# Kernel tuning notes

Hardware: AMD Instinct MI355X
Metric: run time of the kernel (lower is better)

The kernel has to match this reference:

```python
import jax, jax.numpy as jnp
import numpy as np

T, B, IN = 64, 4096, 145
H1, H2 = 150, 32


def _lstm_layer(x, w_ih, w_hh, b_ih, b_hh):
    """Single LSTM layer, PyTorch gate order (i, f, g, o).
    x: (T, B, in_dim); w_ih: (4H, in_dim); w_hh: (4H, H); biases: (4H,).
    Returns hidden sequence (T, B, H)."""
    H = w_hh.shape[1]
    Bsz = x.shape[1]
    # Precompute input contribution for all timesteps at once (one big GEMM).
    xg = jnp.einsum('tbi,gi->tbg', x, w_ih) + (b_ih + b_hh)  # (T, B, 4H)
    w_hh_t = w_hh.T  # (H, 4H)

    def step(carry, xg_t):
        h, c = carry
        gates = xg_t + h @ w_hh_t  # (B, 4H)
        i, f, g, o = jnp.split(gates, 4, axis=-1)
        i = jax.nn.sigmoid(i)
        f = jax.nn.sigmoid(f)
        g = jnp.tanh(g)
        o = jax.nn.sigmoid(o)
        c = f * c + i * g
        h = o * jnp.tanh(c)
        return (h, c), h

    h0 = jnp.zeros((Bsz, H), x.dtype)
    c0 = jnp.zeros((Bsz, H), x.dtype)
    _, hs = jax.lax.scan(step, (h0, c0), xg)
    return hs  # (T, B, H)


def _init_lstm_params(key, in_dim, hidden):
    # PyTorch init: U(-k, k) with k = 1/sqrt(hidden)
    k = 1.0 / np.sqrt(hidden)
    ks = jax.random.split(key, 4)
    w_ih = jax.random.uniform(ks[0], (4 * hidden, in_dim), jnp.float32, -k, k)
    w_hh = jax.random.uniform(ks[1], (4 * hidden, hidden), jnp.float32, -k, k)
    b_ih = jax.random.uniform(ks[2], (4 * hidden,), jnp.float32, -k, k)
    b_hh = jax.random.uniform(ks[3], (4 * hidden,), jnp.float32, -k, k)
    return w_ih, w_hh, b_ih, b_hh


def setup_inputs() -> dict:
    key = jax.random.key(0)
    kx, k0, k1, k2 = jax.random.split(key, 4)
    x = jax.random.normal(kx, (T, B, IN), jnp.float32)
    w_ih_l0, w_hh_l0, b_ih_l0, b_hh_l0 = _init_lstm_params(k0, IN, H1)
    w_ih_l1, w_hh_l1, b_ih_l1, b_hh_l1 = _init_lstm_params(k1, H1, H1)
    w_ih_l2, w_hh_l2, b_ih_l2, b_hh_l2 = _init_lstm_params(k2, H1, H2)
    return {
        'x': x,
        'w_ih_l0': w_ih_l0, 'w_hh_l0': w_hh_l0, 'b_ih_l0': b_ih_l0, 'b_hh_l0': b_hh_l0,
        'w_ih_l1': w_ih_l1, 'w_hh_l1': w_hh_l1, 'b_ih_l1': b_ih_l1, 'b_hh_l1': b_hh_l1,
        'w_ih_l2': w_ih_l2, 'w_hh_l2': w_hh_l2, 'b_ih_l2': b_ih_l2, 'b_hh_l2': b_hh_l2,
    }


def reference(x,
              w_ih_l0, w_hh_l0, b_ih_l0, b_hh_l0,
              w_ih_l1, w_hh_l1, b_ih_l1, b_hh_l1,
              w_ih_l2, w_hh_l2, b_ih_l2, b_hh_l2):
    # temporal_model1: 2-layer LSTM (145 -> 150 -> 150)
    h = _lstm_layer(x, w_ih_l0, w_hh_l0, b_ih_l0, b_hh_l0)
    h = _lstm_layer(h, w_ih_l1, w_hh_l1, b_ih_l1, b_hh_l1)
    # temporal_model2: 1-layer LSTM (150 -> 32)
    out2 = _lstm_layer(h, w_ih_l2, w_hh_l2, b_ih_l2, b_hh_l2)
    return out2  # (T, B, 32)
```

## Files before the change

### kernel.cpp

```cpp
#include <hip/hip_runtime.h>


typedef _Float16 f16;
typedef _Float16 f16x8 __attribute__((ext_vector_type(8)));
typedef float f32x4 __attribute__((ext_vector_type(4)));

#define T_STEPS 64
#define BATCH 4096

__device__ __forceinline__ float sigf(float x) { return 1.0f / (1.0f + __expf(-x)); }
__device__ __forceinline__ float tanh_f(float x) {
  float e = __expf(2.0f * x);
  return 1.0f - 2.0f / (e + 1.0f);
}

#define BAR_LGKM() asm volatile("s_waitcnt lgkmcnt(0)\n\ts_barrier" ::: "memory")

#define PIN_FRAG(w) asm volatile("" : "+v"(*reinterpret_cast<f32x4*>(&(w))))

template <int IN_DIM, int H, int MODE>
__global__ __attribute__((amdgpu_waves_per_eu(2, 2))) __launch_bounds__(512) void lstm_layer(
    const float* __restrict__ xin_f32, const f16* __restrict__ xin_f16,
    const float* __restrict__ w_ih, const float* __restrict__ w_hh,
    const float* __restrict__ b_ih, const float* __restrict__ b_hh,
    f16* __restrict__ hout, float* __restrict__ yout) {
  constexpr int KX = (IN_DIM + 31) / 32;
  constexpr int XPAD = KX * 32;
  constexpr int XSTR = XPAD + 8;
  constexpr int KH = (H + 31) / 32;
  constexpr int HSTR = KH * 32 + 8;
  constexpr int NPAD = ((H + 31) / 32) * 32;
  constexpr int NT = NPAD / 32;
  constexpr int GROUPS = NPAD * 4;
  constexpr int UPD_ITERS = (GROUPS + 511) / 512;
  constexpr int XIN_ELEMS = 16 * IN_DIM;
  constexpr int QX = (XIN_ELEMS + 511) / 512;
  constexpr int STG = (16 * XSTR) / 8;
  constexpr int HCP = (16 * HSTR) / 8;
  static_assert(MODE == 0 || XSTR == 168, "ws stride must match LDS stride");
  static_assert(MODE == 2 || HSTR == 168, "h tile must match ws stride");

  __shared__ __align__(16) f16 xbuf[2][16 * XSTR];
  __shared__ __align__(16) f16 hbuf[16 * HSTR];
  __shared__ __align__(16) float gates[NPAD * 84];

  const int tid = threadIdx.x;
  const int l = tid & 63;
  const int wv = tid >> 6;
  const int gate = wv >> 1;
  const int half = wv & 1;
  const int lrow = l & 15;
  const int lk8 = (l >> 4) * 8;
  const int r0 = (l >> 4) * 4;
  const int b0 = blockIdx.x * 16;

  {
    f16* xf = &xbuf[0][0];
    for (int i = tid; i < 2 * 16 * XSTR; i += 512) xf[i] = (f16)0.f;
    for (int i = tid; i < 16 * HSTR; i += 512) hbuf[i] = (f16)0.f;
  }

  const int rbase = half * (NPAD / 2) + lrow;
  float bias_reg[NT];
#pragma unroll
  for (int nt = 0; nt < NT; ++nt) {
    int n = rbase + nt * 16;
    bias_reg[nt] = (n < H) ? (b_ih[gate * H + n] + b_hh[gate * H + n]) : 0.f;
  }

  f16x8 wx[KX][NT], wh[KH][NT];
#pragma unroll
  for (int kc = 0; kc < KX; ++kc)
#pragma unroll
    for (int nt = 0; nt < NT; ++nt) {
      f16x8 w;
#pragma unroll
      for (int j = 0; j < 8; ++j) {
        int k = kc * 32 + lk8 + j;
        int r = rbase + nt * 16;
        float v = (r < H && k < IN_DIM) ? w_ih[(size_t)(gate * H + r) * IN_DIM + k] : 0.f;
        w[j] = (f16)v;
      }
      wx[kc][nt] = w;
      PIN_FRAG(wx[kc][nt]);
    }
#pragma unroll
  for (int kc = 0; kc < KH; ++kc)
#pragma unroll
    for (int nt = 0; nt < NT; ++nt) {
      f16x8 w;
#pragma unroll
      for (int j = 0; j < 8; ++j) {
        int k = kc * 32 + lk8 + j;
        int r = rbase + nt * 16;
        float v = (r < H && k < H) ? w_hh[(size_t)(gate * H + r) * H + k] : 0.f;
        w[j] = (f16)v;
      }
      wh[kc][nt] = w;
      PIN_FRAG(wh[kc][nt]);
    }

  if constexpr (MODE == 0) {
#pragma unroll
    for (int q = 0; q < QX; ++q) {
      int idx = q * 512 + tid;
      if (idx < XIN_ELEMS) {
        float v = xin_f32[(size_t)b0 * IN_DIM + idx];
        int r = idx / IN_DIM, c = idx - r * IN_DIM;
        xbuf[0][r * XSTR + c] = (f16)v;
      }
    }
  } else {
    if (tid < STG) {
      f16x8 v = *(const f16x8*)(xin_f16 + (size_t)b0 * 168 + tid * 8);
      *(f16x8*)(&xbuf[0][tid * 8]) = v;
    }
  }
  __syncthreads();

  float creg[UPD_ITERS][4];
#pragma unroll
  for (int it = 0; it < UPD_ITERS; ++it)
#pragma unroll
    for (int j = 0; j < 4; ++j) creg[it][j] = 0.f;

  float xv[QX];
  f16x8 pv;

  for (int t = 0; t < T_STEPS; ++t) {
    const int cur = t & 1, nxt = cur ^ 1;

    if (t + 1 < T_STEPS) {
      if constexpr (MODE == 0) {
        const float* src = xin_f32 + ((size_t)(t + 1) * BATCH + b0) * IN_DIM;
#pragma unroll
        for (int q = 0; q < QX; ++q) {
          int idx = q * 512 + tid;
          xv[q] = (idx < XIN_ELEMS) ? src[idx] : 0.f;
        }
      } else {
        if (tid < STG)
          pv = *(const f16x8*)(xin_f16 + ((size_t)(t + 1) * BATCH + b0) * 168 + tid * 8);
      }
    }

    if constexpr (MODE != 2) {
      if (t > 0 && tid < HCP) {
        f16x8 v = *(const f16x8*)(&hbuf[tid * 8]);
        *(f16x8*)(hout + ((size_t)(t - 1) * BATCH + b0) * 168 + tid * 8) = v;
      }
    }

    f32x4 acc[NT];
#pragma unroll
    for (int nt = 0; nt < NT; ++nt) {
      float b = bias_reg[nt];
      acc[nt] = f32x4{b, b, b, b};
    }
    {
      const f16* xb = &xbuf[cur][0];
#pragma unroll
      for (int kc = 0; kc < KX; ++kc) {
        f16x8 a = *(const f16x8*)(xb + lrow * XSTR + kc * 32 + lk8);
#pragma unroll
        for (int nt = 0; nt < NT; ++nt)
          acc[nt] = __builtin_amdgcn_mfma_f32_16x16x32_f16(a, wx[kc][nt], acc[nt], 0, 0, 0);
      }
#pragma unroll
      for (int kc = 0; kc < KH; ++kc) {
        f16x8 a = *(const f16x8*)(hbuf + lrow * HSTR + kc * 32 + lk8);
#pragma unroll
        for (int nt = 0; nt < NT; ++nt)
          acc[nt] = __builtin_amdgcn_mfma_f32_16x16x32_f16(a, wh[kc][nt], acc[nt], 0, 0, 0);
      }
    }
#pragma unroll
    for (int nt = 0; nt < NT; ++nt) {
      int n = half * (NPAD / 2) + nt * 16 + lrow;
      *(f32x4*)(&gates[n * 84 + gate * 20 + r0]) = acc[nt];
    }

    BAR_LGKM();

    if (t + 1 < T_STEPS) {
      if constexpr (MODE == 0) {
#pragma unroll
        for (int q = 0; q < QX; ++q) {
          int idx = q * 512 + tid;
          if (idx < XIN_ELEMS) {
            int r = idx / IN_DIM, c = idx - r * IN_DIM;
            xbuf[nxt][r * XSTR + c] = (f16)xv[q];
          }
        }
      } else {
        if (tid < STG) *(f16x8*)(&xbuf[nxt][tid * 8]) = pv;
      }
    }

#pragma unroll
    for (int it = 0; it < UPD_ITERS; ++it) {
      int grp = it * 512 + tid;
      if (grp < GROUPS) {
        int n = grp % NPAD;
        int rb = (grp / NPAD) * 4;
        if (n < H) {
          f32x4 gi = *(const f32x4*)(&gates[n * 84 + 0 + rb]);
          f32x4 gf = *(const f32x4*)(&gates[n * 84 + 20 + rb]);
          f32x4 gg = *(const f32x4*)(&gates[n * 84 + 40 + rb]);
          f32x4 go = *(const f32x4*)(&gates[n * 84 + 60 + rb]);
#pragma unroll
          for (int j = 0; j < 4; ++j) {
            float iv = sigf(gi[j]);
            float fv = sigf(gf[j]);
            float gv = tanh_f(gg[j]);
            float ov = sigf(go[j]);
            float c = fv * creg[it][j] + iv * gv;
            creg[it][j] = c;
            float h = ov * tanh_f(c);
            hbuf[(rb + j) * HSTR + n] = (f16)h;
            if constexpr (MODE == 2) {
              yout[((size_t)t * BATCH + b0 + rb + j) * 32 + n] = h;
            }
          }
        }
      }
    }

    BAR_LGKM();
  }

  if constexpr (MODE != 2) {
    if (tid < HCP) {
      f16x8 v = *(const f16x8*)(&hbuf[tid * 8]);
      *(f16x8*)(hout + ((size_t)(T_STEPS - 1) * BATCH + b0) * 168 + tid * 8) = v;
    }
  }
}

extern "C" void kernel_launch(void* const* d_in, const int* in_sizes, int n_in,
                              void* d_out, int out_size, void* d_ws, size_t ws_size,
                              hipStream_t stream) {
  const float* x = (const float*)d_in[0];
  const float* wih0 = (const float*)d_in[1];
  const float* whh0 = (const float*)d_in[2];
  const float* bih0 = (const float*)d_in[3];
  const float* bhh0 = (const float*)d_in[4];
  const float* wih1 = (const float*)d_in[5];
  const float* whh1 = (const float*)d_in[6];
  const float* bih1 = (const float*)d_in[7];
  const float* bhh1 = (const float*)d_in[8];
  const float* wih2 = (const float*)d_in[9];
  const float* whh2 = (const float*)d_in[10];
  const float* bih2 = (const float*)d_in[11];
  const float* bhh2 = (const float*)d_in[12];

  f16* hws = (f16*)d_ws;
  float* out = (float*)d_out;

  dim3 grid(BATCH / 16), block(512);
  lstm_layer<145, 150, 0><<<grid, block, 0, stream>>>(x, nullptr, wih0, whh0, bih0, bhh0, hws, nullptr);
  lstm_layer<150, 150, 1><<<grid, block, 0, stream>>>(nullptr, hws, wih1, whh1, bih1, bhh1, hws, nullptr);
  lstm_layer<150, 32, 2><<<grid, block, 0, stream>>>(nullptr, hws, wih2, whh2, bih2, bhh2, nullptr, out);
}
```

Baseline: 686.4 us.

## Split big LSTM layers into hoisted input GEMM plus lean recurrent kernel

For the two H=150 layers, the input projection for all timesteps is now computed by a separate parallel GEMM kernel that writes f16 gate preactivations with bias into workspace. A new recurrent kernel with 640 threads holds only W_hh in registers, one wave per 16 output columns covering all four gates. This lets it do the gate nonlinearity directly from accumulators without an LDS gates round-trip and with one barrier per step. The trade is extra global traffic for the xg buffer, and f16 rounding of gate preactivations. The path runs only if the workspace is large enough, otherwise it falls back to the old kernels.

```diff
diff --git a/kernel.cpp b/kernel.cpp
--- a/kernel.cpp
+++ b/kernel.cpp
@@ -3,6 +3,7 @@
 
 typedef _Float16 f16;
 typedef _Float16 f16x8 __attribute__((ext_vector_type(8)));
+typedef _Float16 f16x4 __attribute__((ext_vector_type(4)));
 typedef float f32x4 __attribute__((ext_vector_type(4)));
 
 #define T_STEPS 64
@@ -16,17 +17,170 @@
 
 #define BAR_LGKM() asm volatile("s_waitcnt lgkmcnt(0)\n\ts_barrier" ::: "memory")
 
-#define PIN_FRAG(w) asm volatile("" : "+v"(*reinterpret_cast<f32x4*>(&(w))))
+template <int IN_DIM, int SRC_F16>
+__global__ __launch_bounds__(512) void gemm_xg(
+    const float* __restrict__ xin_f32, const f16* __restrict__ xin_f16,
+    const float* __restrict__ w_ih, const float* __restrict__ b_ih,
+    const float* __restrict__ b_hh, f16* __restrict__ xg) {
+  constexpr int ASTR = 168, H = 150, NPG = 160, CPAD = 640, NTG = 10;
+  __shared__ __align__(16) f16 A_lds[128 * ASTR];
+  __shared__ __align__(16) f16 W_lds[64 * ASTR];
+  __shared__ float bias_lds[64];
+  const int tid = threadIdx.x;
+  const int ntile = blockIdx.x % NTG, mtile = blockIdx.x / NTG;
+  const int g0 = mtile * 128;
+  const int n0 = ntile * 64;
+
+  if constexpr (SRC_F16) {
+    const f16* src = xin_f16 + (size_t)g0 * 168;
+#pragma unroll
+    for (int q = 0; q < 6; ++q) {
+      int idx = q * 512 + tid;
+      if (idx < 128 * 21) *(f16x8*)(&A_lds[idx * 8]) = *(const f16x8*)(src + (size_t)idx * 8);
+    }
+  } else {
+#pragma unroll
+    for (int q = 0; q < 42; ++q) {
+      int idx = q * 512 + tid;
+      int r = idx / ASTR, c = idx - r * ASTR;
+      float v = (c < IN_DIM) ? xin_f32[(size_t)(g0 + r) * IN_DIM + c] : 0.f;
+      A_lds[idx] = (f16)v;
+    }
+  }
+#pragma unroll
+  for (int q = 0; q < 21; ++q) {
+    int idx = q * 512 + tid;
+    int i = idx / ASTR, k = idx - i * ASTR;
+    int c = n0 + i, gate = c / NPG, cg = c - gate * NPG;
+    float v = (cg < H && k < IN_DIM) ? w_ih[(size_t)(gate * H + cg) * IN_DIM + k] : 0.f;
+    W_lds[idx] = (f16)v;
+  }
+  if (tid < 64) {
+    int c = n0 + tid, gate = c / NPG, cg = c - gate * NPG;
+    bias_lds[tid] = (cg < H) ? (b_ih[gate * H + cg] + b_hh[gate * H + cg]) : 0.f;
+  }
+  __syncthreads();
+
+  const int l = tid & 63, wv = tid >> 6;
+  const int lrow = l & 15, lk8 = (l >> 4) * 8, r0 = (l >> 4) * 4;
+  f32x4 acc[4];
+#pragma unroll
+  for (int nt = 0; nt < 4; ++nt) acc[nt] = f32x4{0.f, 0.f, 0.f, 0.f};
+#pragma unroll
+  for (int kc = 0; kc < 5; ++kc) {
+    f16x8 a = *(const f16x8*)(&A_lds[(wv * 16 + lrow) * ASTR + kc * 32 + lk8]);
+#pragma unroll
+    for (int nt = 0; nt < 4; ++nt) {
+      f16x8 b = *(const f16x8*)(&W_lds[(nt * 16 + lrow) * ASTR + kc * 32 + lk8]);
+      acc[nt] = __builtin_amdgcn_mfma_f32_16x16x32_f16(a, b, acc[nt], 0, 0, 0);
+    }
+  }
+  const size_t wgb = (size_t)(g0 / 16 + wv);
+#pragma unroll
+  for (int nt = 0; nt < 4; ++nt) {
+    int cl = nt * 16 + lrow;
+    float bs = bias_lds[cl];
+    f16x4 o;
+#pragma unroll
+    for (int j = 0; j < 4; ++j) o[j] = (f16)(acc[nt][j] + bs);
+    *(f16x4*)(xg + (wgb * CPAD + n0 + cl) * 16 + r0) = o;
+  }
+}
+
+__global__ __launch_bounds__(640, 2) void lstm_rec(
+    const f16* __restrict__ xg, const float* __restrict__ whh,
+    f16* __restrict__ hout) {
+  constexpr int H = 150, HSTR = 168, CPAD = 640;
+  __shared__ __align__(16) f16 hbuf[2][16 * HSTR];
+  const int tid = threadIdx.x;
+  const int l = tid & 63, w = tid >> 6;
+  const int lrow = l & 15, lk8 = (l >> 4) * 8, r0 = (l >> 4) * 4;
+  const int col = w * 16 + lrow;
+  const int bx = blockIdx.x, b0 = bx * 16;
+
+  for (int i = tid; i < 2 * 16 * HSTR / 8; i += 640) {
+    f16x8 z = {};
+    *(f16x8*)(&hbuf[0][0] + (size_t)i * 8) = z;
+  }
+
+  f16x8 wh[4][5];
+#pragma unroll
+  for (int g = 0; g < 4; ++g)
+#pragma unroll
+    for (int kc = 0; kc < 5; ++kc) {
+      f16x8 v;
+#pragma unroll
+      for (int j = 0; j < 8; ++j) {
+        int k = kc * 32 + lk8 + j;
+        float x = (col < H && k < H) ? whh[((size_t)g * H + col) * H + k] : 0.f;
+        v[j] = (f16)x;
+      }
+      wh[g][kc] = v;
+    }
+  __syncthreads();
+
+  float creg[4] = {0.f, 0.f, 0.f, 0.f};
+  f16x4 pv[4];
+#pragma unroll
+  for (int g = 0; g < 4; ++g)
+    pv[g] = *(const f16x4*)(xg + ((size_t)bx * CPAD + g * 160 + col) * 16 + r0);
+
+  for (int t = 0; t < T_STEPS; ++t) {
+    const int cur = t & 1, nxt = cur ^ 1;
+
+    if (t > 0 && tid < 336) {
+      f16x8 v = *(const f16x8*)(&hbuf[cur][tid * 8]);
+      *(f16x8*)(hout + ((size_t)(t - 1) * BATCH + b0) * 168 + (size_t)tid * 8) = v;
+    }
+
+    f32x4 acc[4];
+#pragma unroll
+    for (int g = 0; g < 4; ++g) {
+#pragma unroll
+      for (int j = 0; j < 4; ++j) acc[g][j] = (float)pv[g][j];
+    }
+    if (t + 1 < T_STEPS) {
+#pragma unroll
+      for (int g = 0; g < 4; ++g)
+        pv[g] = *(const f16x4*)(xg + ((size_t)((t + 1) * 256 + bx) * CPAD + g * 160 + col) * 16 + r0);
+    }
+
+#pragma unroll
+    for (int kc = 0; kc < 5; ++kc) {
+      f16x8 a = *(const f16x8*)(&hbuf[cur][lrow * HSTR + kc * 32 + lk8]);
+#pragma unroll
+      for (int g = 0; g < 4; ++g)
+        acc[g] = __builtin_amdgcn_mfma_f32_16x16x32_f16(a, wh[g][kc], acc[g], 0, 0, 0);
+    }
+
+#pragma unroll
+    for (int j = 0; j < 4; ++j) {
+      float iv = sigf(acc[0][j]);
+      float fv = sigf(acc[1][j]);
+      float gv = tanh_f(acc[2][j]);
+      float ov = sigf(acc[3][j]);
+      float c = fv * creg[j] + iv * gv;
+      creg[j] = c;
+      float h = ov * tanh_f(c);
+      hbuf[nxt][(r0 + j) * HSTR + col] = (f16)h;
+    }
+
+    BAR_LGKM();
+  }
+  if (tid < 336) {
+    f16x8 v = *(const f16x8*)(&hbuf[0][tid * 8]);
+    *(f16x8*)(hout + ((size_t)(T_STEPS - 1) * BATCH + b0) * 168 + (size_t)tid * 8) = v;
+  }
+}
 
 template <int IN_DIM, int H, int MODE>
-__global__ __attribute__((amdgpu_waves_per_eu(2, 2))) __launch_bounds__(512) void lstm_layer(
+__global__ __launch_bounds__(512, 2) void lstm_layer(
     const float* __restrict__ xin_f32, const f16* __restrict__ xin_f16,
     const float* __restrict__ w_ih, const float* __restrict__ w_hh,
     const float* __restrict__ b_ih, const float* __restrict__ b_hh,
     f16* __restrict__ hout, float* __restrict__ yout) {
   constexpr int KX = (IN_DIM + 31) / 32;
-  constexpr int XPAD = KX * 32;
-  constexpr int XSTR = XPAD + 8;
+  constexpr int XSTR = KX * 32 + 8;
   constexpr int KH = (H + 31) / 32;
   constexpr int HSTR = KH * 32 + 8;
   constexpr int NPAD = ((H + 31) / 32) * 32;
@@ -37,8 +191,7 @@
   constexpr int QX = (XIN_ELEMS + 511) / 512;
   constexpr int STG = (16 * XSTR) / 8;
   constexpr int HCP = (16 * HSTR) / 8;
-  static_assert(MODE == 0 || XSTR == 168, "ws stride must match LDS stride");
-  static_assert(MODE == 2 || HSTR == 168, "h tile must match ws stride");
+  static_assert(MODE == 0 || XSTR == 168, "");
 
   __shared__ __align__(16) f16 xbuf[2][16 * XSTR];
   __shared__ __align__(16) f16 hbuf[16 * HSTR];
@@ -59,7 +212,6 @@
     for (int i = tid; i < 2 * 16 * XSTR; i += 512) xf[i] = (f16)0.f;
     for (int i = tid; i < 16 * HSTR; i += 512) hbuf[i] = (f16)0.f;
   }
-
   const int rbase = half * (NPAD / 2) + lrow;
   float bias_reg[NT];
 #pragma unroll
@@ -67,37 +219,34 @@
     int n = rbase + nt * 16;
     bias_reg[nt] = (n < H) ? (b_ih[gate * H + n] + b_hh[gate * H + n]) : 0.f;
   }
-
   f16x8 wx[KX][NT], wh[KH][NT];
 #pragma unroll
   for (int kc = 0; kc < KX; ++kc)
 #pragma unroll
     for (int nt = 0; nt < NT; ++nt) {
-      f16x8 w;
+      f16x8 wq;
 #pragma unroll
       for (int j = 0; j < 8; ++j) {
         int k = kc * 32 + lk8 + j;
         int r = rbase + nt * 16;
         float v = (r < H && k < IN_DIM) ? w_ih[(size_t)(gate * H + r) * IN_DIM + k] : 0.f;
-        w[j] = (f16)v;
-      }
-      wx[kc][nt] = w;
-      PIN_FRAG(wx[kc][nt]);
+        wq[j] = (f16)v;
+      }
+      wx[kc][nt] = wq;
     }
 #pragma unroll
   for (int kc = 0; kc < KH; ++kc)
 #pragma unroll
     for (int nt = 0; nt < NT; ++nt) {
-      f16x8 w;
+      f16x8 wq;
 #pragma unroll
       for (int j = 0; j < 8; ++j) {
         int k = kc * 32 + lk8 + j;
         int r = rbase + nt * 16;
         float v = (r < H && k < H) ? w_hh[(size_t)(gate * H + r) * H + k] : 0.f;
-        w[j] = (f16)v;
-      }
-      wh[kc][nt] = w;
-      PIN_FRAG(wh[kc][nt]);
+        wq[j] = (f16)v;
+      }
+      wh[kc][nt] = wq;
     }
 
   if constexpr (MODE == 0) {
@@ -129,7 +278,6 @@
 
   for (int t = 0; t < T_STEPS; ++t) {
     const int cur = t & 1, nxt = cur ^ 1;
-
     if (t + 1 < T_STEPS) {
       if constexpr (MODE == 0) {
         const float* src = xin_f32 + ((size_t)(t + 1) * BATCH + b0) * IN_DIM;
@@ -143,14 +291,12 @@
           pv = *(const f16x8*)(xin_f16 + ((size_t)(t + 1) * BATCH + b0) * 168 + tid * 8);
       }
     }
-
     if constexpr (MODE != 2) {
       if (t > 0 && tid < HCP) {
         f16x8 v = *(const f16x8*)(&hbuf[tid * 8]);
         *(f16x8*)(hout + ((size_t)(t - 1) * BATCH + b0) * 168 + tid * 8) = v;
       }
     }
-
     f32x4 acc[NT];
 #pragma unroll
     for (int nt = 0; nt < NT; ++nt) {
@@ -179,9 +325,7 @@
       int n = half * (NPAD / 2) + nt * 16 + lrow;
       *(f32x4*)(&gates[n * 84 + gate * 20 + r0]) = acc[nt];
     }
-
     BAR_LGKM();
-
     if (t + 1 < T_STEPS) {
       if constexpr (MODE == 0) {
 #pragma unroll
@@ -196,7 +340,6 @@
         if (tid < STG) *(f16x8*)(&xbuf[nxt][tid * 8]) = pv;
       }
     }
-
 #pragma unroll
     for (int it = 0; it < UPD_ITERS; ++it) {
       int grp = it * 512 + tid;
@@ -225,10 +368,8 @@
         }
       }
     }
-
     BAR_LGKM();
   }
-
   if constexpr (MODE != 2) {
     if (tid < HCP) {
       f16x8 v = *(const f16x8*)(&hbuf[tid * 8]);
@@ -254,11 +395,25 @@
   const float* bih2 = (const float*)d_in[11];
   const float* bhh2 = (const float*)d_in[12];
 
+  const size_t HSEQ_BYTES = (size_t)T_STEPS * BATCH * 168 * sizeof(f16);
+  const size_t XG_BYTES = (size_t)T_STEPS * BATCH * 640 * sizeof(f16);
   f16* hws = (f16*)d_ws;
   float* out = (float*)d_out;
 
-  dim3 grid(BATCH / 16), block(512);
-  lstm_layer<145, 150, 0><<<grid, block, 0, stream>>>(x, nullptr, wih0, whh0, bih0, bhh0, hws, nullptr);
-  lstm_layer<150, 150, 1><<<grid, block, 0, stream>>>(nullptr, hws, wih1, whh1, bih1, bhh1, hws, nullptr);
-  lstm_layer<150, 32, 2><<<grid, block, 0, stream>>>(nullptr, hws, wih2, whh2, bih2, bhh2, nullptr, out);
+  if (ws_size >= HSEQ_BYTES + XG_BYTES) {
+    f16* xgbuf = (f16*)((char*)d_ws + HSEQ_BYTES);
+    dim3 gg(20480), gb(512);
+    dim3 rg(BATCH / 16), rb(640);
+    gemm_xg<145, 0><<<gg, gb, 0, stream>>>(x, nullptr, wih0, bih0, bhh0, xgbuf);
+    lstm_rec<<<rg, rb, 0, stream>>>(xgbuf, whh0, hws);
+    gemm_xg<150, 1><<<gg, gb, 0, stream>>>(nullptr, hws, wih1, bih1, bhh1, xgbuf);
+    lstm_rec<<<rg, rb, 0, stream>>>(xgbuf, whh1, hws);
+    lstm_layer<150, 32, 2><<<dim3(BATCH / 16), dim3(512), 0, stream>>>(
+        nullptr, hws, wih2, whh2, bih2, bhh2, nullptr, out);
+  } else {
+    dim3 grid(BATCH / 16), block(512);
+    lstm_layer<145, 150, 0><<<grid, block, 0, stream>>>(x, nullptr, wih0, whh0, bih0, bhh0, hws, nullptr);
+    lstm_layer<150, 150, 1><<<grid, block, 0, stream>>>(nullptr, hws, wih1, whh1, bih1, bhh1, hws, nullptr);
+    lstm_layer<150, 32, 2><<<grid, block, 0, stream>>>(nullptr, hws, wih2, whh2, bih2, bhh2, nullptr, out);
+  }
 }
```

New measurement: 1.787 ms. 160% more time.
